# Kernel tuning notes

Hardware: AMD Instinct MI355X
Metric: run time of the kernel (lower is better)

## Reference

```python
import jax, jax.numpy as jnp
import numpy as np

D = 1024  # q_dim == k_dim == v_dim
B, QL, KL = 8, 2048, 2048
NEG_BIG = -1e12  # matches torch masked_fill_(-1000000000000.0)


def setup_inputs() -> dict:
    key = jax.random.key(0)
    kq, kk, kv, kp = jax.random.split(key, 4)
    Q = jax.random.normal(kq, (B, QL, D), dtype=jnp.float32)
    K = jax.random.normal(kk, (B, KL, D), dtype=jnp.float32)
    V = jax.random.normal(kv, (B, KL, D), dtype=jnp.float32)
    attn_mask = jnp.zeros((QL, KL), dtype=jnp.float32)
    key_pad_mask = jax.random.randint(kp, (B, KL), 0, 2).astype(jnp.bool_)
    return {"Q": Q, "K": K, "V": V, "attn_mask": attn_mask, "key_pad_mask": key_pad_mask}


def reference(Q, K, V, attn_mask, key_pad_mask):
    temperature = jnp.asarray(np.sqrt(D), dtype=Q.dtype)
    # [B, QL, KL] scores: dot mode
    scores = jnp.einsum("bqd,bkd->bqk", Q, K) / temperature
    scores = scores + attn_mask[None, :, :]
    scores = jnp.where(key_pad_mask[:, None, :], NEG_BIG, scores)
    attn_weights = jax.nn.softmax(scores, axis=-1)  # dropout p=0 -> identity
    attn_ctx = jnp.einsum("bqk,bkd->bqd", attn_weights, V)
    return attn_ctx, attn_weights
```

## Files before the change

### kernel.cpp

```cpp
#include <hip/hip_runtime.h>
#include <hip/hip_fp16.h>

#define B_ 8
#define QL_ 2048
#define KL_ 2048
#define D_ 1024

typedef _Float16 f16x8 __attribute__((ext_vector_type(8)));
typedef _Float16 f16x4 __attribute__((ext_vector_type(4)));
typedef float f32x4 __attribute__((ext_vector_type(4)));

__device__ __forceinline__ void async16(const void* g, void* l) {
  __builtin_amdgcn_global_load_lds(
      (const __attribute__((address_space(1))) unsigned int*)g,
      (__attribute__((address_space(3))) unsigned int*)l, 16, 0, 0);
}

__global__ __launch_bounds__(256) void prep_k(const int* __restrict__ pad,
                                              int* __restrict__ pos,
                                              int* __restrict__ inv,
                                              int* __restrict__ kcp) {
  const int b = blockIdx.x;
  const int t = threadIdx.x;
  const int lane = t & 63, wv = t >> 6;
  __shared__ int wsum[4], wpre[4], kc_sh;
  const int* pr = pad + b * KL_;
  int* po = pos + b * KL_;
  int* iv = inv + b * KL_;
  int c[8], loc = 0;
#pragma unroll
  for (int j = 0; j < 8; ++j) {
    c[j] = (pr[t * 8 + j] == 0);
    loc += c[j];
  }
  int inc = loc;
  for (int d = 1; d < 64; d <<= 1) {
    int v = __shfl_up(inc, d);
    if (lane >= d) inc += v;
  }
  if (lane == 63) wsum[wv] = inc;
  __syncthreads();
  if (t == 0) {
    int acc = 0;
    for (int w = 0; w < 4; ++w) {
      wpre[w] = acc;
      acc += wsum[w];
    }
    kc_sh = acc;
    kcp[b] = (acc == 0) ? KL_ : acc;
  }
  __syncthreads();
  const int kc = kc_sh;
  int base = wpre[wv] + inc - loc;
#pragma unroll
  for (int j = 0; j < 8; ++j) {
    const int k = t * 8 + j;
    if (kc == 0) {
      po[k] = k;
      iv[k] = k;
    } else {
      po[k] = base;
      if (c[j]) iv[base] = k;
    }
    base += c[j];
  }
}

__global__ __launch_bounds__(256) void cvtvt_k(
    const float* __restrict__ Q, const float* __restrict__ K,
    const float* __restrict__ V, _Float16* __restrict__ Qh,
    _Float16* __restrict__ Khc, _Float16* __restrict__ VTc,
    const int* __restrict__ pad, const int* __restrict__ pos) {
  constexpr int CVT = B_ * QL_ * D_ / 8 / 256;
  __shared__ float tile[32][33];
  const int id = blockIdx.x;
  if (id < 2 * CVT) {
    const bool isQ = id < CVT;
    const int i = (isQ ? id : id - CVT) * 256 + threadIdx.x;
    const float4* src = reinterpret_cast<const float4*>(isQ ? Q : K);
    const float scale = isQ ? 0.03125f : 1.0f;
    float4 a = src[i * 2], b = src[i * 2 + 1];
    f16x8 h;
    h[0] = (_Float16)(a.x * scale); h[1] = (_Float16)(a.y * scale);
    h[2] = (_Float16)(a.z * scale); h[3] = (_Float16)(a.w * scale);
    h[4] = (_Float16)(b.x * scale); h[5] = (_Float16)(b.y * scale);
    h[6] = (_Float16)(b.z * scale); h[7] = (_Float16)(b.w * scale);
    if (isQ) {
      reinterpret_cast<f16x8*>(Qh)[i] = h;
    } else {
      const int gk = (i * 8) >> 10;
      const int col8 = i & 127;
      if (pad[gk] == 0) {
        const int b2 = gk >> 11;
        const int prow = pos[gk];
        reinterpret_cast<f16x8*>(Khc)[(size_t)(b2 << 11 | prow) * 128 + col8] =
            h;
      }
    }
  } else {
    const int vid = id - 2 * CVT;
    const int k0 = (vid & 63) * 32;
    const int d0 = ((vid >> 6) & 31) * 32;
    const int b = vid >> 11;
    const float* Vb = V + (size_t)b * KL_ * D_;
    _Float16* VTb = VTc + (size_t)b * D_ * KL_;
    const int c = threadIdx.x & 31, r = threadIdx.x >> 5;
#pragma unroll
    for (int s = 0; s < 4; ++s)
      tile[r + s * 8][c] = Vb[(size_t)(k0 + r + s * 8) * D_ + d0 + c];
    __syncthreads();
    const int kk = k0 + c;
    const int keep = (pad[b * KL_ + kk] == 0);
    const int col = pos[b * KL_ + kk];
#pragma unroll
    for (int s = 0; s < 4; ++s)
      if (keep)
        VTb[(size_t)(d0 + r + s * 8) * KL_ + col] =
            (_Float16)tile[c][r + s * 8];
  }
}

__global__ __launch_bounds__(256) void cvt2_k(const float* __restrict__ Q,
                                              const float* __restrict__ K,
                                              _Float16* __restrict__ Qh,
                                              _Float16* __restrict__ Kh) {
  constexpr int HALF = B_ * QL_ * D_ / 8 / 256;
  const bool isQ = blockIdx.x < HALF;
  const int i = (isQ ? blockIdx.x : blockIdx.x - HALF) * 256 + threadIdx.x;
  const float4* src = reinterpret_cast<const float4*>(isQ ? Q : K);
  const float scale = isQ ? 0.03125f : 1.0f;
  float4 a = src[i * 2], b = src[i * 2 + 1];
  f16x8 h;
  h[0] = (_Float16)(a.x * scale); h[1] = (_Float16)(a.y * scale);
  h[2] = (_Float16)(a.z * scale); h[3] = (_Float16)(a.w * scale);
  h[4] = (_Float16)(b.x * scale); h[5] = (_Float16)(b.y * scale);
  h[6] = (_Float16)(b.z * scale); h[7] = (_Float16)(b.w * scale);
  reinterpret_cast<f16x8*>(isQ ? Qh : Kh)[i] = h;
}

__global__ __launch_bounds__(256) void vt_k(const float* __restrict__ V,
                                            _Float16* __restrict__ VT) {
  __shared__ float tile[32][33];
  const int k0 = blockIdx.x * 32, d0 = blockIdx.y * 32, b = blockIdx.z;
  const float* Vb = V + (size_t)b * KL_ * D_;
  _Float16* VTb = VT + (size_t)b * D_ * KL_;
  const int c = threadIdx.x & 31, r = threadIdx.x >> 5;
#pragma unroll
  for (int s = 0; s < 4; ++s)
    tile[r + s * 8][c] = Vb[(size_t)(k0 + r + s * 8) * D_ + d0 + c];
  __syncthreads();
#pragma unroll
  for (int s = 0; s < 4; ++s)
    VTb[(size_t)(d0 + r + s * 8) * KL_ + k0 + c] = (_Float16)tile[c][r + s * 8];
}

template <bool SCORES>
__global__ __launch_bounds__(512, 2) void fgemm_k(
    const _Float16* __restrict__ Ah, const _Float16* __restrict__ Bh,
    float* __restrict__ Cf, _Float16* __restrict__ Ch) {
  constexpr int Mc = 2048;
  constexpr int Nc = SCORES ? 2048 : 1024;
  constexpr int Kc = SCORES ? 1024 : 2048;
  constexpr int NIT = Kc / 64;
  constexpr int GX = Mc / 256, GY = Nc / 256;
  constexpr int CPX = B_ * GX * GY / 8;

  extern __shared__ char lds[];

  const int t = threadIdx.x;
  const int lane = t & 63;
  const int wid = t >> 6;
  const int wr = wid >> 2, wc = wid & 3;
  const int lo = lane & 15, hi = lane >> 4;

  const int id = blockIdx.x;
  const int swz = (id & 7) * CPX + (id >> 3);
  const int b = swz / (GX * GY);
  const int rem = swz % (GX * GY);
  const int m0 = (rem / GY) * 256, n0 = (rem % GY) * 256;

  const _Float16* Ab = Ah + (size_t)b * Mc * Kc;
  const _Float16* Bb = Bh + (size_t)b * Nc * Kc;

  int aoff[4], boff[4], ldst[4];
#pragma unroll
  for (int j = 0; j < 4; ++j) {
    const int row = j * 64 + wid * 8 + (lane >> 3);
    const int cg = (lane & 7) ^ (lane >> 3);
    aoff[j] = (m0 + row) * Kc + cg * 8;
    boff[j] = (n0 + row) * Kc + cg * 8;
    ldst[j] = j * 8192 + wid * 1024;
  }

  auto stage = [&](int it, int slot) {
    char* base = lds + slot * 65536;
    const int kb = it * 64;
#pragma unroll
    for (int j = 0; j < 4; ++j) {
      async16(Ab + aoff[j] + kb, base + ldst[j]);
      async16(Bb + boff[j] + kb, base + 32768 + ldst[j]);
    }
  };

  f32x4 acc[8][4];
#pragma unroll
  for (int m = 0; m < 8; ++m)
#pragma unroll
    for (int n = 0; n < 4; ++n)
#pragma unroll
      for (int i = 0; i < 4; ++i) acc[m][n][i] = 0.0f;

  int raf[8], rbf_[4];
#pragma unroll
  for (int m = 0; m < 8; ++m) {
    const int r = wr * 128 + m * 16 + lo;
    raf[m] = r * 128 + ((hi ^ (r & 7)) << 4);
  }
#pragma unroll
  for (int n = 0; n < 4; ++n) {
    const int r = wc * 64 + n * 16 + lo;
    rbf_[n] = r * 128 + ((hi ^ (r & 7)) << 4);
  }

  auto compute = [&](int slot) {
    const char* Ac = lds + slot * 65536;
    const char* Bc = Ac + 32768;
#pragma unroll
    for (int kh = 0; kh < 2; ++kh) {
      const int kx = kh * 64;
      f16x8 af[8], bfr[4];
#pragma unroll
      for (int m = 0; m < 8; ++m)
        af[m] = *reinterpret_cast<const f16x8*>(Ac + (raf[m] ^ kx));
#pragma unroll
      for (int n = 0; n < 4; ++n)
        bfr[n] = *reinterpret_cast<const f16x8*>(Bc + (rbf_[n] ^ kx));
      __builtin_amdgcn_s_setprio(1);
#pragma unroll
      for (int m = 0; m < 8; ++m)
#pragma unroll
        for (int n = 0; n < 4; ++n)
          acc[m][n] = __builtin_amdgcn_mfma_f32_16x16x32_f16(
              af[m], bfr[n], acc[m][n], 0, 0, 0);
      __builtin_amdgcn_s_setprio(0);
      __builtin_amdgcn_sched_barrier(0);
    }
  };

  stage(0, 0);
  for (int it = 0; it < NIT; ++it) {
    asm volatile("s_waitcnt vmcnt(0) lgkmcnt(0)" ::: "memory");
    __builtin_amdgcn_sched_barrier(0);
    __builtin_amdgcn_s_barrier();
    if (it + 1 < NIT) stage(it + 1, (it + 1) & 1);
    compute(it & 1);
  }

  if constexpr (SCORES) {
    _Float16* Cb = Ch + (size_t)b * Mc * Nc;
#pragma unroll
    for (int n = 0; n < 4; ++n) {
      const int col = n0 + wc * 64 + n * 16 + lo;
#pragma unroll
      for (int m = 0; m < 8; ++m) {
        const int r0 = m0 + wr * 128 + m * 16 + hi * 4;
#pragma unroll
        for (int i = 0; i < 4; ++i)
          Cb[(size_t)(r0 + i) * Nc + col] = (_Float16)acc[m][n][i];
      }
    }
  } else {
    float* Cb = Cf + (size_t)b * Mc * Nc;
#pragma unroll
    for (int n = 0; n < 4; ++n) {
      const int col = n0 + wc * 64 + n * 16 + lo;
#pragma unroll
      for (int m = 0; m < 8; ++m) {
        const int r0 = m0 + wr * 128 + m * 16 + hi * 4;
#pragma unroll
        for (int i = 0; i < 4; ++i)
          Cb[(size_t)(r0 + i) * Nc + col] = acc[m][n][i];
      }
    }
  }
}

__global__ __launch_bounds__(512, 2) void fgemm_qkc(
    const _Float16* __restrict__ Qh, const _Float16* __restrict__ Khc,
    _Float16* __restrict__ Sh, const int* __restrict__ inv,
    const int* __restrict__ kcp) {
  constexpr int Mc = 2048, Nc = 2048, Kc = 1024;
  constexpr int NIT = Kc / 64;

  extern __shared__ char lds[];

  const int t = threadIdx.x;
  const int lane = t & 63;
  const int wid = t >> 6;
  const int wr = wid >> 2, wc = wid & 3;
  const int lo = lane & 15, hi = lane >> 4;

  const int id = blockIdx.x;
  const int b = id & 7;
  const int nl = (id >> 3) & 3;
  const int m = (id >> 5) & 7;
  const int nh = (id >> 8) & 1;
  const int m0 = m * 256;
  const int n0 = (nh * 4 + nl) * 256;

  const int kc = kcp[b];
  if (n0 >= ((kc + 63) & ~63)) return;

  const _Float16* Ab = Qh + (size_t)b * Mc * Kc;
  const _Float16* Bb = Khc + (size_t)b * Nc * Kc;

  int aoff[4], boff[4], ldst[4];
#pragma unroll
  for (int j = 0; j < 4; ++j) {
    const int row = j * 64 + wid * 8 + (lane >> 3);
    const int cg = (lane & 7) ^ (lane >> 3);
    aoff[j] = (m0 + row) * Kc + cg * 8;
    boff[j] = (n0 + row) * Kc + cg * 8;
    ldst[j] = j * 8192 + wid * 1024;
  }

  auto stage = [&](int it, int slot) {
    char* base = lds + slot * 65536;
    const int kb = it * 64;
#pragma unroll
    for (int j = 0; j < 4; ++j) {
      async16(Ab + aoff[j] + kb, base + ldst[j]);
      async16(Bb + boff[j] + kb, base + 32768 + ldst[j]);
    }
  };

  f32x4 acc[8][4];
#pragma unroll
  for (int m2 = 0; m2 < 8; ++m2)
#pragma unroll
    for (int n = 0; n < 4; ++n)
#pragma unroll
      for (int i = 0; i < 4; ++i) acc[m2][n][i] = 0.0f;

  int raf[8], rbf_[4];
#pragma unroll
  for (int m2 = 0; m2 < 8; ++m2) {
    const int r = wr * 128 + m2 * 16 + lo;
    raf[m2] = r * 128 + ((hi ^ (r & 7)) << 4);
  }
#pragma unroll
  for (int n = 0; n < 4; ++n) {
    const int r = wc * 64 + n * 16 + lo;
    rbf_[n] = r * 128 + ((hi ^ (r & 7)) << 4);
  }

  auto compute = [&](int slot) {
    const char* Ac = lds + slot * 65536;
    const char* Bc = Ac + 32768;
#pragma unroll
    for (int kh = 0; kh < 2; ++kh) {
      const int kx = kh * 64;
      f16x8 af[8], bfr[4];
#pragma unroll
      for (int m2 = 0; m2 < 8; ++m2)
        af[m2] = *reinterpret_cast<const f16x8*>(Ac + (raf[m2] ^ kx));
#pragma unroll
      for (int n = 0; n < 4; ++n)
        bfr[n] = *reinterpret_cast<const f16x8*>(Bc + (rbf_[n] ^ kx));
      __builtin_amdgcn_s_setprio(1);
#pragma unroll
      for (int m2 = 0; m2 < 8; ++m2)
#pragma unroll
        for (int n = 0; n < 4; ++n)
          acc[m2][n] = __builtin_amdgcn_mfma_f32_16x16x32_f16(
              af[m2], bfr[n], acc[m2][n], 0, 0, 0);
      __builtin_amdgcn_s_setprio(0);
      __builtin_amdgcn_sched_barrier(0);
    }
  };

  stage(0, 0);
  for (int it = 0; it < NIT; ++it) {
    asm volatile("s_waitcnt vmcnt(0) lgkmcnt(0)" ::: "memory");
    __builtin_amdgcn_sched_barrier(0);
    __builtin_amdgcn_s_barrier();
    if (it + 1 < NIT) stage(it + 1, (it + 1) & 1);
    compute(it & 1);
  }

  _Float16* Cb = Sh + (size_t)b * Mc * Nc;
  const int* ivb = inv + b * KL_;
#pragma unroll
  for (int n = 0; n < 4; ++n) {
    const int ccol = n0 + wc * 64 + n * 16 + lo;
    if (ccol < kc) {
      const int dcol = ivb[ccol];
#pragma unroll
      for (int m2 = 0; m2 < 8; ++m2) {
        const int r0 = m0 + wr * 128 + m2 * 16 + hi * 4;
#pragma unroll
        for (int i = 0; i < 4; ++i)
          Cb[(size_t)(r0 + i) * Nc + dcol] = (_Float16)acc[m2][n][i];
      }
    }
  }
}

__global__ __launch_bounds__(512, 2) void fgemm_pv(
    const _Float16* __restrict__ Whc, const _Float16* __restrict__ VTc,
    float* __restrict__ Cf, const int* __restrict__ kcp) {
  constexpr int Mc = 2048, Nc = 1024;
  constexpr int GX = 8, GY = 4;
  constexpr int CPX = B_ * GX * GY / 8;

  extern __shared__ char lds[];

  const int t = threadIdx.x;
  const int lane = t & 63;
  const int wid = t >> 6;
  const int wr = wid >> 2, wc = wid & 3;
  const int lo = lane & 15, hi = lane >> 4;

  const int id = blockIdx.x;
  const int swz = (id & 7) * CPX + (id >> 3);
  const int b = swz / (GX * GY);
  const int rem = swz % (GX * GY);
  const int m0 = (rem / GY) * 256, n0 = (rem % GY) * 256;

  const int kc = kcp[b];
  const int KA = (kc + 63) & ~63;
  const int NIT = KA >> 6;

  const _Float16* Ab = Whc + (size_t)b * 2048 * 2048;
  const _Float16* Bb = VTc + (size_t)b * Nc * KL_;

  int aoff[4], boff[4], ldst[4];
#pragma unroll
  for (int j = 0; j < 4; ++j) {
    const int row = j * 64 + wid * 8 + (lane >> 3);
    const int cg = (lane & 7) ^ (lane >> 3);
    aoff[j] = (m0 + row) * KA + cg * 8;
    boff[j] = (n0 + row) * KL_ + cg * 8;
    ldst[j] = j * 8192 + wid * 1024;
  }

  auto stage = [&](int it, int slot) {
    char* base = lds + slot * 65536;
    const int kb = it * 64;
#pragma unroll
    for (int j = 0; j < 4; ++j) {
      async16(Ab + aoff[j] + kb, base + ldst[j]);
      async16(Bb + boff[j] + kb, base + 32768 + ldst[j]);
    }
  };

  f32x4 acc[8][4];
#pragma unroll
  for (int m = 0; m < 8; ++m)
#pragma unroll
    for (int n = 0; n < 4; ++n)
#pragma unroll
      for (int i = 0; i < 4; ++i) acc[m][n][i] = 0.0f;

  int raf[8], rbf_[4];
#pragma unroll
  for (int m = 0; m < 8; ++m) {
    const int r = wr * 128 + m * 16 + lo;
    raf[m] = r * 128 + ((hi ^ (r & 7)) << 4);
  }
#pragma unroll
  for (int n = 0; n < 4; ++n) {
    const int r = wc * 64 + n * 16 + lo;
    rbf_[n] = r * 128 + ((hi ^ (r & 7)) << 4);
  }

  auto compute = [&](int slot) {
    const char* Ac = lds + slot * 65536;
    const char* Bc = Ac + 32768;
#pragma unroll
    for (int kh = 0; kh < 2; ++kh) {
      const int kx = kh * 64;
      f16x8 af[8], bfr[4];
#pragma unroll
      for (int m = 0; m < 8; ++m)
        af[m] = *reinterpret_cast<const f16x8*>(Ac + (raf[m] ^ kx));
#pragma unroll
      for (int n = 0; n < 4; ++n)
        bfr[n] = *reinterpret_cast<const f16x8*>(Bc + (rbf_[n] ^ kx));
      __builtin_amdgcn_s_setprio(1);
#pragma unroll
      for (int m = 0; m < 8; ++m)
#pragma unroll
        for (int n = 0; n < 4; ++n)
          acc[m][n] = __builtin_amdgcn_mfma_f32_16x16x32_f16(
              af[m], bfr[n], acc[m][n], 0, 0, 0);
      __builtin_amdgcn_s_setprio(0);
      __builtin_amdgcn_sched_barrier(0);
    }
  };

  stage(0, 0);
  for (int it = 0; it < NIT; ++it) {
    asm volatile("s_waitcnt vmcnt(0) lgkmcnt(0)" ::: "memory");
    __builtin_amdgcn_sched_barrier(0);
    __builtin_amdgcn_s_barrier();
    if (it + 1 < NIT) stage(it + 1, (it + 1) & 1);
    compute(it & 1);
  }

  float* Cb = Cf + (size_t)b * Mc * Nc;
#pragma unroll
  for (int n = 0; n < 4; ++n) {
    const int col = n0 + wc * 64 + n * 16 + lo;
#pragma unroll
    for (int m = 0; m < 8; ++m) {
      const int r0 = m0 + wr * 128 + m * 16 + hi * 4;
#pragma unroll
      for (int i = 0; i < 4; ++i)
        Cb[(size_t)(r0 + i) * Nc + col] = acc[m][n][i];
    }
  }
}

template <bool COMPACT>
__global__ __launch_bounds__(256) void softmax_k(
    const _Float16* __restrict__ Sh, float* __restrict__ W,
    _Float16* __restrict__ Wh, const float* __restrict__ mask,
    const int* __restrict__ pad, const int* __restrict__ pos,
    const int* __restrict__ kcp) {
  const int row = blockIdx.x * 4 + (threadIdx.x >> 6);
  const int lane = threadIdx.x & 63;
  const int b = row >> 11, q = row & 2047;
  const f16x4* Sr = reinterpret_cast<const f16x4*>(Sh + (size_t)row * KL_);
  float4* Wr = reinterpret_cast<float4*>(W + (size_t)row * KL_);
  const float4* Mr = reinterpret_cast<const float4*>(mask + (size_t)q * KL_);
  const int4* Pr = reinterpret_cast<const int4*>(pad + (size_t)b * KL_);
  int4 pk[8];
  float4 v[8];
#pragma unroll
  for (int s = 0; s < 8; ++s) {
    f16x4 sv = Sr[s * 64 + lane];
    float4 mk = Mr[s * 64 + lane];
    int4 p = Pr[s * 64 + lane];
    pk[s] = p;
    float4 x;
    x.x = p.x ? -1e12f : (float)sv[0] + mk.x;
    x.y = p.y ? -1e12f : (float)sv[1] + mk.y;
    x.z = p.z ? -1e12f : (float)sv[2] + mk.z;
    x.w = p.w ? -1e12f : (float)sv[3] + mk.w;
    v[s] = x;
  }
  float mx = -3.402823466e38f;
#pragma unroll
  for (int s = 0; s < 8; ++s)
    mx = fmaxf(mx, fmaxf(fmaxf(v[s].x, v[s].y), fmaxf(v[s].z, v[s].w)));
#pragma unroll
  for (int off = 32; off > 0; off >>= 1) mx = fmaxf(mx, __shfl_xor(mx, off));
  float sum = 0.0f;
#pragma unroll
  for (int s = 0; s < 8; ++s) {
    v[s].x = __expf(v[s].x - mx);
    v[s].y = __expf(v[s].y - mx);
    v[s].z = __expf(v[s].z - mx);
    v[s].w = __expf(v[s].w - mx);
    sum += v[s].x + v[s].y + v[s].z + v[s].w;
  }
#pragma unroll
  for (int off = 32; off > 0; off >>= 1) sum += __shfl_xor(sum, off);
  const float inv = 1.0f / sum;

  if constexpr (COMPACT) {
    const int kc = kcp[b];
    const int kcpad = (kc + 63) & ~63;
    _Float16* Wc = Wh + (size_t)b * 2048 * 2048 + (size_t)q * kcpad;
    const int4* Po = reinterpret_cast<const int4*>(pos + (size_t)b * KL_);
#pragma unroll
    for (int s = 0; s < 8; ++s) {
      float4 o;
      o.x = v[s].x * inv;
      o.y = v[s].y * inv;
      o.z = v[s].z * inv;
      o.w = v[s].w * inv;
      Wr[s * 64 + lane] = o;
      int4 ps = Po[s * 64 + lane];
      if (!pk[s].x) Wc[ps.x] = (_Float16)o.x;
      if (!pk[s].y) Wc[ps.y] = (_Float16)o.y;
      if (!pk[s].z) Wc[ps.z] = (_Float16)o.z;
      if (!pk[s].w) Wc[ps.w] = (_Float16)o.w;
    }
    if (kc + lane < kcpad) Wc[kc + lane] = (_Float16)0.0f;
  } else {
    f16x4* Whr = reinterpret_cast<f16x4*>(Wh + (size_t)row * KL_);
#pragma unroll
    for (int s = 0; s < 8; ++s) {
      float4 o;
      o.x = v[s].x * inv;
      o.y = v[s].y * inv;
      o.z = v[s].z * inv;
      o.w = v[s].w * inv;
      Wr[s * 64 + lane] = o;
      f16x4 h;
      h[0] = (_Float16)o.x;
      h[1] = (_Float16)o.y;
      h[2] = (_Float16)o.z;
      h[3] = (_Float16)o.w;
      Whr[s * 64 + lane] = h;
    }
  }
}

extern "C" void kernel_launch(void* const* d_in, const int* in_sizes, int n_in,
                              void* d_out, int out_size, void* d_ws,
                              size_t ws_size, hipStream_t stream) {
  const float* Q = (const float*)d_in[0];
  const float* K = (const float*)d_in[1];
  const float* V = (const float*)d_in[2];
  const float* mask = (const float*)d_in[3];
  const int* pad = (const int*)d_in[4];

  float* ctx = (float*)d_out;
  float* W = ctx + (size_t)B_ * QL_ * D_;
  _Float16* Sh = (_Float16*)d_out;

  const size_t MB = 1024 * 1024;
  _Float16* VT = (_Float16*)d_ws;
  _Float16* Qh = (_Float16*)((char*)d_ws + 32 * MB);
  _Float16* Kh = (_Float16*)((char*)d_ws + 64 * MB);
  _Float16* Wh = Qh;

  (void)hipFuncSetAttribute((const void*)fgemm_k<true>,
                            hipFuncAttributeMaxDynamicSharedMemorySize, 131072);
  (void)hipFuncSetAttribute((const void*)fgemm_k<false>,
                            hipFuncAttributeMaxDynamicSharedMemorySize, 131072);
  (void)hipFuncSetAttribute((const void*)fgemm_qkc,
                            hipFuncAttributeMaxDynamicSharedMemorySize, 131072);
  (void)hipFuncSetAttribute((const void*)fgemm_pv,
                            hipFuncAttributeMaxDynamicSharedMemorySize, 131072);

  const bool compact = ws_size >= 96 * MB + (1 << 18);
  if (compact) {
    int* pos = (int*)((char*)d_ws + 96 * MB);
    int* inv = pos + B_ * KL_;
    int* kcp = inv + B_ * KL_;
    prep_k<<<dim3(B_), 256, 0, stream>>>(pad, pos, inv, kcp);
    cvtvt_k<<<dim3(2 * 8192 + 64 * 32 * B_), 256, 0, stream>>>(
        Q, K, V, Qh, Kh, VT, pad, pos);
    fgemm_qkc<<<dim3(B_ * 8 * 8), 512, 131072, stream>>>(Qh, Kh, Sh, inv, kcp);
    softmax_k<true><<<dim3(B_ * QL_ / 4), 256, 0, stream>>>(Sh, W, Wh, mask,
                                                            pad, pos, kcp);
    fgemm_pv<<<dim3(B_ * 8 * 4), 512, 131072, stream>>>(Wh, VT, ctx, kcp);
  } else {
    cvt2_k<<<dim3(2 * B_ * QL_ * D_ / 8 / 256), 256, 0, stream>>>(Q, K, Qh, Kh);
    vt_k<<<dim3(KL_ / 32, D_ / 32, B_), 256, 0, stream>>>(V, VT);
    fgemm_k<true><<<dim3(B_ * 8 * 8), 512, 131072, stream>>>(Qh, Kh, nullptr,
                                                             Sh);
    softmax_k<false><<<dim3(B_ * QL_ / 4), 256, 0, stream>>>(
        Sh, W, Wh, mask, pad, nullptr, nullptr);
    fgemm_k<false><<<dim3(B_ * 8 * 4), 512, 131072, stream>>>(Wh, VT, ctx,
                                                              nullptr);
  }
}
```

Baseline: 242.2 us.

## Split QK^T GEMM into big tiles for first half, small tiles for ragged tail

The compacted QK^T kernel now handles the first 1024 compacted key columns with 256x256 tiles and the remaining columns with 128x64 tiles in extra blocks. Because compacted key counts sit near half of the keys, the goal is to reduce wasted work and tail imbalance from large tiles that are only partially used past the boundary. The small tiles have lower arithmetic intensity and less reuse, and the launch still reserves 128KB LDS per block while using only 64KB in the tail path, which may limit occupancy.

```diff
diff --git a/kernel.cpp b/kernel.cpp
--- a/kernel.cpp
+++ b/kernel.cpp
@@ -289,7 +289,7 @@
     const _Float16* __restrict__ Qh, const _Float16* __restrict__ Khc,
     _Float16* __restrict__ Sh, const int* __restrict__ inv,
     const int* __restrict__ kcp) {
-  constexpr int Mc = 2048, Nc = 2048, Kc = 1024;
+  constexpr int Kc = 1024;
   constexpr int NIT = Kc / 64;
 
   extern __shared__ char lds[];
@@ -297,110 +297,200 @@
   const int t = threadIdx.x;
   const int lane = t & 63;
   const int wid = t >> 6;
-  const int wr = wid >> 2, wc = wid & 3;
   const int lo = lane & 15, hi = lane >> 4;
-
   const int id = blockIdx.x;
-  const int b = id & 7;
-  const int nl = (id >> 3) & 3;
-  const int m = (id >> 5) & 7;
-  const int nh = (id >> 8) & 1;
-  const int m0 = m * 256;
-  const int n0 = (nh * 4 + nl) * 256;
-
-  const int kc = kcp[b];
-  if (n0 >= ((kc + 63) & ~63)) return;
-
-  const _Float16* Ab = Qh + (size_t)b * Mc * Kc;
-  const _Float16* Bb = Khc + (size_t)b * Nc * Kc;
-
-  int aoff[4], boff[4], ldst[4];
-#pragma unroll
-  for (int j = 0; j < 4; ++j) {
-    const int row = j * 64 + wid * 8 + (lane >> 3);
+
+  if (id < 256) {
+    const int wr = wid >> 2, wc = wid & 3;
+    const int b = id & 7;
+    const int n0 = ((id >> 3) & 3) * 256;
+    const int m0 = ((id >> 5) & 7) * 256;
+
+    const int kc = kcp[b];
+    if (n0 >= ((kc + 63) & ~63)) return;
+
+    const _Float16* Ab = Qh + (size_t)b * 2048 * Kc;
+    const _Float16* Bb = Khc + (size_t)b * 2048 * Kc;
+
+    int aoff[4], boff[4], ldst[4];
+#pragma unroll
+    for (int j = 0; j < 4; ++j) {
+      const int row = j * 64 + wid * 8 + (lane >> 3);
+      const int cg = (lane & 7) ^ (lane >> 3);
+      aoff[j] = (m0 + row) * Kc + cg * 8;
+      boff[j] = (n0 + row) * Kc + cg * 8;
+      ldst[j] = j * 8192 + wid * 1024;
+    }
+
+    auto stage = [&](int it, int slot) {
+      char* base = lds + slot * 65536;
+      const int kb = it * 64;
+#pragma unroll
+      for (int j = 0; j < 4; ++j) {
+        async16(Ab + aoff[j] + kb, base + ldst[j]);
+        async16(Bb + boff[j] + kb, base + 32768 + ldst[j]);
+      }
+    };
+
+    f32x4 acc[8][4];
+#pragma unroll
+    for (int m2 = 0; m2 < 8; ++m2)
+#pragma unroll
+      for (int n = 0; n < 4; ++n)
+#pragma unroll
+        for (int i = 0; i < 4; ++i) acc[m2][n][i] = 0.0f;
+
+    int raf[8], rbf_[4];
+#pragma unroll
+    for (int m2 = 0; m2 < 8; ++m2) {
+      const int r = wr * 128 + m2 * 16 + lo;
+      raf[m2] = r * 128 + ((hi ^ (r & 7)) << 4);
+    }
+#pragma unroll
+    for (int n = 0; n < 4; ++n) {
+      const int r = wc * 64 + n * 16 + lo;
+      rbf_[n] = r * 128 + ((hi ^ (r & 7)) << 4);
+    }
+
+    auto compute = [&](int slot) {
+      const char* Ac = lds + slot * 65536;
+      const char* Bc = Ac + 32768;
+#pragma unroll
+      for (int kh = 0; kh < 2; ++kh) {
+        const int kx = kh * 64;
+        f16x8 af[8], bfr[4];
+#pragma unroll
+        for (int m2 = 0; m2 < 8; ++m2)
+          af[m2] = *reinterpret_cast<const f16x8*>(Ac + (raf[m2] ^ kx));
+#pragma unroll
+        for (int n = 0; n < 4; ++n)
+          bfr[n] = *reinterpret_cast<const f16x8*>(Bc + (rbf_[n] ^ kx));
+        __builtin_amdgcn_s_setprio(1);
+#pragma unroll
+        for (int m2 = 0; m2 < 8; ++m2)
+#pragma unroll
+          for (int n = 0; n < 4; ++n)
+            acc[m2][n] = __builtin_amdgcn_mfma_f32_16x16x32_f16(
+                af[m2], bfr[n], acc[m2][n], 0, 0, 0);
+        __builtin_amdgcn_s_setprio(0);
+        __builtin_amdgcn_sched_barrier(0);
+      }
+    };
+
+    stage(0, 0);
+    for (int it = 0; it < NIT; ++it) {
+      asm volatile("s_waitcnt vmcnt(0) lgkmcnt(0)" ::: "memory");
+      __builtin_amdgcn_sched_barrier(0);
+      __builtin_amdgcn_s_barrier();
+      if (it + 1 < NIT) stage(it + 1, (it + 1) & 1);
+      compute(it & 1);
+    }
+
+    _Float16* Cb = Sh + (size_t)b * 2048 * 2048;
+    const int* ivb = inv + b * KL_;
+#pragma unroll
+    for (int n = 0; n < 4; ++n) {
+      const int ccol = n0 + wc * 64 + n * 16 + lo;
+      if (ccol < kc) {
+        const int dcol = ivb[ccol];
+#pragma unroll
+        for (int m2 = 0; m2 < 8; ++m2) {
+          const int r0 = m0 + wr * 128 + m2 * 16 + hi * 4;
+#pragma unroll
+          for (int i = 0; i < 4; ++i)
+            Cb[(size_t)(r0 + i) * 2048 + dcol] = (_Float16)acc[m2][n][i];
+        }
+      }
+    }
+  } else {
+    const int tid = id - 256;
+    const int b = tid & 7;
+    const int m0 = ((tid >> 3) & 15) * 128;
+    const int n0 = 1024 + ((tid >> 7) & 15) * 64;
+
+    const int kc = kcp[b];
+    if (n0 >= ((kc + 63) & ~63)) return;
+
+    const _Float16* Ab = Qh + (size_t)b * 2048 * Kc;
+    const _Float16* Bb = Khc + (size_t)b * 2048 * Kc;
+
     const int cg = (lane & 7) ^ (lane >> 3);
-    aoff[j] = (m0 + row) * Kc + cg * 8;
-    boff[j] = (n0 + row) * Kc + cg * 8;
-    ldst[j] = j * 8192 + wid * 1024;
-  }
-
-  auto stage = [&](int it, int slot) {
-    char* base = lds + slot * 65536;
-    const int kb = it * 64;
-#pragma unroll
-    for (int j = 0; j < 4; ++j) {
-      async16(Ab + aoff[j] + kb, base + ldst[j]);
-      async16(Bb + boff[j] + kb, base + 32768 + ldst[j]);
-    }
-  };
-
-  f32x4 acc[8][4];
-#pragma unroll
-  for (int m2 = 0; m2 < 8; ++m2)
+    int aoff[2], ldstA[2];
+#pragma unroll
+    for (int j = 0; j < 2; ++j) {
+      const int row = j * 64 + wid * 8 + (lane >> 3);
+      aoff[j] = (m0 + row) * Kc + cg * 8;
+      ldstA[j] = j * 8192 + wid * 1024;
+    }
+    const int boff0 = (n0 + wid * 8 + (lane >> 3)) * Kc + cg * 8;
+
+    auto stage = [&](int it, int slot) {
+      char* base = lds + slot * 32768;
+      const int kb = it * 64;
+      async16(Ab + aoff[0] + kb, base + ldstA[0]);
+      async16(Ab + aoff[1] + kb, base + ldstA[1]);
+      async16(Bb + boff0 + kb, base + 16384 + wid * 1024);
+    };
+
+    f32x4 acc[4];
 #pragma unroll
     for (int n = 0; n < 4; ++n)
 #pragma unroll
-      for (int i = 0; i < 4; ++i) acc[m2][n][i] = 0.0f;
-
-  int raf[8], rbf_[4];
-#pragma unroll
-  for (int m2 = 0; m2 < 8; ++m2) {
-    const int r = wr * 128 + m2 * 16 + lo;
-    raf[m2] = r * 128 + ((hi ^ (r & 7)) << 4);
-  }
-#pragma unroll
-  for (int n = 0; n < 4; ++n) {
-    const int r = wc * 64 + n * 16 + lo;
-    rbf_[n] = r * 128 + ((hi ^ (r & 7)) << 4);
-  }
-
-  auto compute = [&](int slot) {
-    const char* Ac = lds + slot * 65536;
-    const char* Bc = Ac + 32768;
-#pragma unroll
-    for (int kh = 0; kh < 2; ++kh) {
-      const int kx = kh * 64;
-      f16x8 af[8], bfr[4];
-#pragma unroll
-      for (int m2 = 0; m2 < 8; ++m2)
-        af[m2] = *reinterpret_cast<const f16x8*>(Ac + (raf[m2] ^ kx));
-#pragma unroll
-      for (int n = 0; n < 4; ++n)
-        bfr[n] = *reinterpret_cast<const f16x8*>(Bc + (rbf_[n] ^ kx));
-      __builtin_amdgcn_s_setprio(1);
-#pragma unroll
-      for (int m2 = 0; m2 < 8; ++m2)
+      for (int i = 0; i < 4; ++i) acc[n][i] = 0.0f;
+
+    int rafm;
+    {
+      const int r = wid * 16 + lo;
+      rafm = r * 128 + ((hi ^ (r & 7)) << 4);
+    }
+    int rbf2[4];
+#pragma unroll
+    for (int n = 0; n < 4; ++n) {
+      const int r = n * 16 + lo;
+      rbf2[n] = r * 128 + ((hi ^ (r & 7)) << 4);
+    }
+
+    auto compute = [&](int slot) {
+      const char* Ac = lds + slot * 32768;
+      const char* Bc = Ac + 16384;
+#pragma unroll
+      for (int kh = 0; kh < 2; ++kh) {
+        const int kx = kh * 64;
+        f16x8 af = *reinterpret_cast<const f16x8*>(Ac + (rafm ^ kx));
+        f16x8 bfr[4];
 #pragma unroll
         for (int n = 0; n < 4; ++n)
-          acc[m2][n] = __builtin_amdgcn_mfma_f32_16x16x32_f16(
-              af[m2], bfr[n], acc[m2][n], 0, 0, 0);
-      __builtin_amdgcn_s_setprio(0);
+          bfr[n] = *reinterpret_cast<const f16x8*>(Bc + (rbf2[n] ^ kx));
+        __builtin_amdgcn_s_setprio(1);
+#pragma unroll
+        for (int n = 0; n < 4; ++n)
+          acc[n] = __builtin_amdgcn_mfma_f32_16x16x32_f16(af, bfr[n], acc[n],
+                                                          0, 0, 0);
+        __builtin_amdgcn_s_setprio(0);
+        __builtin_amdgcn_sched_barrier(0);
+      }
+    };
+
+    stage(0, 0);
+    for (int it = 0; it < NIT; ++it) {
+      asm volatile("s_waitcnt vmcnt(0) lgkmcnt(0)" ::: "memory");
       __builtin_amdgcn_sched_barrier(0);
-    }
-  };
-
-  stage(0, 0);
-  for (int it = 0; it < NIT; ++it) {
-    asm volatile("s_waitcnt vmcnt(0) lgkmcnt(0)" ::: "memory");
-    __builtin_amdgcn_sched_barrier(0);
-    __builtin_amdgcn_s_barrier();
-    if (it + 1 < NIT) stage(it + 1, (it + 1) & 1);
-    compute(it & 1);
-  }
-
-  _Float16* Cb = Sh + (size_t)b * Mc * Nc;
-  const int* ivb = inv + b * KL_;
-#pragma unroll
-  for (int n = 0; n < 4; ++n) {
-    const int ccol = n0 + wc * 64 + n * 16 + lo;
-    if (ccol < kc) {
-      const int dcol = ivb[ccol];
-#pragma unroll
-      for (int m2 = 0; m2 < 8; ++m2) {
-        const int r0 = m0 + wr * 128 + m2 * 16 + hi * 4;
+      __builtin_amdgcn_s_barrier();
+      if (it + 1 < NIT) stage(it + 1, (it + 1) & 1);
+      compute(it & 1);
+    }
+
+    _Float16* Cb = Sh + (size_t)b * 2048 * 2048;
+    const int* ivb = inv + b * KL_;
+#pragma unroll
+    for (int n = 0; n < 4; ++n) {
+      const int ccol = n0 + n * 16 + lo;
+      if (ccol < kc) {
+        const int dcol = ivb[ccol];
+        const int r0 = m0 + wid * 16 + hi * 4;
 #pragma unroll
         for (int i = 0; i < 4; ++i)
-          Cb[(size_t)(r0 + i) * Nc + dcol] = (_Float16)acc[m2][n][i];
+          Cb[(size_t)(r0 + i) * 2048 + dcol] = (_Float16)acc[n][i];
       }
     }
   }
@@ -645,7 +735,7 @@
     prep_k<<<dim3(B_), 256, 0, stream>>>(pad, pos, inv, kcp);
     cvtvt_k<<<dim3(2 * 8192 + 64 * 32 * B_), 256, 0, stream>>>(
         Q, K, V, Qh, Kh, VT, pad, pos);
-    fgemm_qkc<<<dim3(B_ * 8 * 8), 512, 131072, stream>>>(Qh, Kh, Sh, inv, kcp);
+    fgemm_qkc<<<dim3(256 + 2048), 512, 131072, stream>>>(Qh, Kh, Sh, inv, kcp);
     softmax_k<true><<<dim3(B_ * QL_ / 4), 256, 0, stream>>>(Sh, W, Wh, mask,
                                                             pad, pos, kcp);
     fgemm_pv<<<dim3(B_ * 8 * 4), 512, 131072, stream>>>(Wh, VT, ctx, kcp);
```

Result: faster. 230.0 us (-5.1%).
